# Kernel optimization log

Measured on AMD Instinct MI355X. Metric: run time of the kernel, lower is better.

## Reference

```python
import jax, jax.numpy as jnp
import numpy as np

B, HC, WC, KC = 4, 32, 32, 1024   # coarse feature map (ResNet101 layer3)
HF, WF, KF = 128, 128, 256        # fine feature map (ResNet101 layer1)
DC = 4                            # downscale_coef; HF // DC == HC


def setup_inputs() -> dict:
    key = jax.random.key(0)
    k1, k2, k3, k4 = jax.random.split(key, 4)
    return {
        "F_g1_coarse": jax.random.normal(k1, (B, HC, WC, KC), jnp.float32),
        "F_gk_coarse": jax.random.normal(k2, (B, HC, WC, KC), jnp.float32),
        "F_g1_fine": jax.random.normal(k3, (B, HF, WF, KF), jnp.float32),
        "F_gk_fine": jax.random.normal(k4, (B, HF, WF, KF), jnp.float32),
    }


def _coarse_match(f1, fk):
    # For every coarse position in Gk find nearest (L2) coarse position in G1.
    b, h, w, k = f1.shape
    a = f1.reshape(b, h * w, k)   # G1 positions
    q = fk.reshape(b, h * w, k)   # Gk positions
    # ||q||^2 + ||a||^2 - 2 q.a  -> [B, HW_gk, HW_g1]
    d = ((q * q).sum(-1)[:, :, None]
         + (a * a).sum(-1)[:, None, :]
         - 2.0 * jnp.einsum('bnk,bmk->bnm', q, a))
    idx = jnp.argmin(d, axis=-1)                       # [B, HW]
    cm = jnp.stack([idx // w, idx % w], axis=-1)       # (row, col) in G1
    return cm.reshape(b, h, w, 2).astype(jnp.int32)


def _fine_match(f1, fk, cm, dc):
    # Refine each dc x dc fine tile of Gk by searching the fine pixels of G1
    # covered by the coarse matches of the 3x3 coarse-neighborhood.
    b, h, w, k = fk.shape
    hc, wc = h // dc, w // dc
    off = jnp.arange(-1, 2)
    nI = jnp.clip(jnp.arange(hc)[:, None] + off[None, :], 0, hc - 1)  # [Hc,3]
    nJ = jnp.clip(jnp.arange(wc)[:, None] + off[None, :], 0, wc - 1)  # [Wc,3]
    # neighbor coarse matches: [B, Hc, Wc, 3, 3, 2]
    nb = cm[:, nI[:, None, :, None], nJ[None, :, None, :]]
    nb = nb.reshape(b, hc, wc, 9, 2)
    # expand each coarse match to its dc*dc fine pixels in G1
    sr = jnp.repeat(jnp.arange(dc), dc)   # [dc^2] row shifts
    sc = jnp.tile(jnp.arange(dc), dc)     # [dc^2] col shifts
    ncand = 9 * dc * dc                   # 144 candidates per tile
    cand_r = (nb[..., 0][..., None] * dc + sr).reshape(b, hc, wc, ncand)
    cand_c = (nb[..., 1][..., None] * dc + sc).reshape(b, hc, wc, ncand)
    # gather candidate fine features from G1: [B, Hc, Wc, N, K]
    bi = jnp.arange(b)[:, None, None, None]
    cand_f = f1[bi, cand_r, cand_c]
    # fine tile features of Gk: [B, Hc, Wc, dc^2, K]
    fkb = fk.reshape(b, hc, dc, wc, dc, k).transpose(0, 1, 3, 2, 4, 5)
    fkb = fkb.reshape(b, hc, wc, dc * dc, k)
    dist = ((fkb * fkb).sum(-1)[..., :, None]
            + (cand_f * cand_f).sum(-1)[..., None, :]
            - 2.0 * jnp.einsum('bhwpk,bhwnk->bhwpn', fkb, cand_f))
    best = jnp.argmin(dist, axis=-1)      # [B, Hc, Wc, dc^2]
    hi = jnp.arange(hc)[None, :, None, None]
    wi = jnp.arange(wc)[None, None, :, None]
    best_r = cand_r[bi, hi, wi, best]     # [B, Hc, Wc, dc^2]
    best_c = cand_c[bi, hi, wi, best]
    def to_grid(x):
        return x.reshape(b, hc, wc, dc, dc).transpose(0, 1, 3, 2, 4).reshape(b, h, w)
    return jnp.stack([to_grid(best_r), to_grid(best_c)], axis=-1).astype(jnp.int32)


def reference(F_g1_coarse, F_gk_coarse, F_g1_fine, F_gk_fine):
    closest_coarse = _coarse_match(F_g1_coarse, F_gk_coarse)   # [B,Hc,Wc,2]
    closest_fine = _fine_match(F_g1_fine, F_gk_fine, closest_coarse, DC)  # [B,H,W,2]
    return closest_coarse, closest_fine
```

## Files before the change

kernel.cpp:

```cpp
#include <hip/hip_runtime.h>
#include <cstdint>
#include <cstddef>

#define BB 4
#define HCC 32
#define WCC 32
#define KCC 1024
#define NCC (HCC*WCC)
#define HFF 128
#define WFF 128
#define KFF 256
#define DCC 4
#define NCHUNK 8

typedef _Float16 half8 __attribute__((ext_vector_type(8)));
typedef _Float16 half4_t __attribute__((ext_vector_type(4)));
typedef float f32x4 __attribute__((ext_vector_type(4)));
#define MFMA16(a,b,c) __builtin_amdgcn_mfma_f32_16x16x32_f16((a),(b),(c),0,0,0)
#define INV2K 0.00048828125f

__device__ inline void cvt8(const float4 u0, const float4 u1, half8& h, half8& l2) {
  float uu[8];
  *(float4*)uu = u0; *(float4*)(uu + 4) = u1;
  #pragma unroll
  for (int e = 0; e < 8; ++e) {
    _Float16 hh = (_Float16)uu[e];
    float r = (uu[e] - (float)hh) * 2048.0f;
    h[e] = hh; l2[e] = (_Float16)r;
  }
}

template<int K>
__global__ __launch_bounds__(256) void preconv_kernel(
    const float* __restrict__ src0, const float* __restrict__ src1,
    _Float16* __restrict__ hi0, _Float16* __restrict__ lo0,
    _Float16* __restrict__ hi1, _Float16* __restrict__ lo1,
    float* __restrict__ nr0, float* __restrict__ nr1, int rows) {
  const float* __restrict__ src = blockIdx.y ? src1 : src0;
  _Float16* __restrict__ hi = blockIdx.y ? hi1 : hi0;
  _Float16* __restrict__ lo = blockIdx.y ? lo1 : lo0;
  float* __restrict__ nrm = blockIdx.y ? nr1 : nr0;
  const int wave = threadIdx.x >> 6, lane = threadIdx.x & 63;
  const int row = blockIdx.x * 4 + wave;
  if (row >= rows) return;
  const float* p = src + (size_t)row * K;
  const size_t ob = (size_t)row * K + lane * 4;
  float s = 0.f;
  #pragma unroll
  for (int c = 0; c < K / 256; ++c) {
    float4 v = *(const float4*)(p + c * 256 + lane * 4);
    s += v.x*v.x + v.y*v.y + v.z*v.z + v.w*v.w;
    float vv[4] = {v.x, v.y, v.z, v.w};
    half4_t h, l2;
    #pragma unroll
    for (int e = 0; e < 4; ++e) {
      _Float16 hh = (_Float16)vv[e];
      l2[e] = (_Float16)((vv[e] - (float)hh) * 2048.0f);
      h[e] = hh;
    }
    *(half4_t*)(hi + ob + c * 256) = h;
    *(half4_t*)(lo + ob + c * 256) = l2;
  }
  #pragma unroll
  for (int m = 1; m <= 32; m <<= 1) s += __shfl_xor(s, m, 64);
  if (lane == 0) nrm[row] = s;
}

__global__ __launch_bounds__(256) void preconv_fine_kernel(
    const float* __restrict__ src, _Float16* __restrict__ hl,
    float* __restrict__ nrm, int rows) {
  const int wave = threadIdx.x >> 6, lane = threadIdx.x & 63;
  const int row = blockIdx.x * 4 + wave;
  if (row >= rows) return;
  float4 v = *(const float4*)(src + (size_t)row * KFF + lane * 4);
  float s = v.x*v.x + v.y*v.y + v.z*v.z + v.w*v.w;
  float vv[4] = {v.x, v.y, v.z, v.w};
  half4_t h, l2;
  #pragma unroll
  for (int e = 0; e < 4; ++e) {
    _Float16 hh = (_Float16)vv[e];
    l2[e] = (_Float16)((vv[e] - (float)hh) * 2048.0f);
    h[e] = hh;
  }
  const size_t dst = (size_t)row * 512 + (lane >> 3) * 64 + ((lane >> 1) & 3) * 16 + (lane & 1) * 4;
  *(half4_t*)(hl + dst)     = h;
  *(half4_t*)(hl + dst + 8) = l2;
  #pragma unroll
  for (int m = 1; m <= 32; m <<= 1) s += __shfl_xor(s, m, 64);
  if (lane == 0) nrm[row] = s;
}

__global__ __launch_bounds__(256) void coarse_kernel3(
    const _Float16* __restrict__ gAhi, const _Float16* __restrict__ gAlo,
    const _Float16* __restrict__ gBhi, const _Float16* __restrict__ gBlo,
    const float* __restrict__ na, const float* __restrict__ nq,
    float* __restrict__ pval, int* __restrict__ pidx) {
  __shared__ _Float16 Ahi[128][64], Alo[128][64];
  __shared__ _Float16 Bhi[64][64],  Blo[64][64];
  __shared__ float a2s[128], q2s[64];
  __shared__ float redv[2][64];
  __shared__ int   redi[2][64];

  const int t = threadIdx.x;
  const int chunk = blockIdx.x;
  const int n0 = blockIdx.y * 64;
  const int b  = blockIdx.z;
  const int m0 = chunk * 128;

  const int ar = t >> 1, ahf = t & 1;
  const int brw = t >> 2, bq = t & 3;
  const int l  = t & 63;
  const int wv = t >> 6;
  const int wm = wv >> 1, wn = wv & 1;

  if (t < 128) a2s[t] = na[b*NCC + m0 + t];
  else if (t < 192) q2s[t - 128] = nq[b*NCC + n0 + (t - 128)];

  const _Float16* __restrict__ gah = gAhi + (size_t)(b*NCC + m0 + ar) * KCC + ahf * 32;
  const _Float16* __restrict__ gal = gAlo + (size_t)(b*NCC + m0 + ar) * KCC + ahf * 32;
  const _Float16* __restrict__ gbh = gBhi + (size_t)(b*NCC + n0 + brw) * KCC + bq * 16;
  const _Float16* __restrict__ gbl = gBlo + (size_t)(b*NCC + n0 + brw) * KCC + bq * 16;

  f32x4 accA[4][2], accB[4][2];
  #pragma unroll
  for (int mt = 0; mt < 4; ++mt)
    #pragma unroll
    for (int nt = 0; nt < 2; ++nt) { accA[mt][nt] = (f32x4)0.f; accB[mt][nt] = (f32x4)0.f; }

  half8 pah[4], pal[4], pbh[2], pbl[2];
  #pragma unroll
  for (int c2 = 0; c2 < 4; ++c2) { pah[c2] = *(const half8*)(gah + c2*8); pal[c2] = *(const half8*)(gal + c2*8); }
  #pragma unroll
  for (int c2 = 0; c2 < 2; ++c2) { pbh[c2] = *(const half8*)(gbh + c2*8); pbl[c2] = *(const half8*)(gbl + c2*8); }

  for (int k0 = 0; k0 < KCC; k0 += 64) {
    __syncthreads();
    #pragma unroll
    for (int c2 = 0; c2 < 4; ++c2) {
      int cs = (ahf * 4 + c2) ^ (ar & 7);
      *(half8*)&Ahi[ar][cs * 8] = pah[c2];
      *(half8*)&Alo[ar][cs * 8] = pal[c2];
    }
    #pragma unroll
    for (int c2 = 0; c2 < 2; ++c2) {
      int cs = (bq * 2 + c2) ^ (brw & 7);
      *(half8*)&Bhi[brw][cs * 8] = pbh[c2];
      *(half8*)&Blo[brw][cs * 8] = pbl[c2];
    }
    __syncthreads();

    if (k0 + 64 < KCC) {
      #pragma unroll
      for (int c2 = 0; c2 < 4; ++c2) {
        pah[c2] = *(const half8*)(gah + k0 + 64 + c2*8);
        pal[c2] = *(const half8*)(gal + k0 + 64 + c2*8);
      }
      #pragma unroll
      for (int c2 = 0; c2 < 2; ++c2) {
        pbh[c2] = *(const half8*)(gbh + k0 + 64 + c2*8);
        pbl[c2] = *(const half8*)(gbl + k0 + 64 + c2*8);
      }
    }

    #pragma unroll
    for (int kk = 0; kk < 2; ++kk) {
      const int cs = ((kk * 4 + (l >> 4)) ^ (l & 7)) * 8;
      half8 ah[4], al[4], bh[2], bl[2];
      #pragma unroll
      for (int mt = 0; mt < 4; ++mt) {
        int row = wm * 64 + mt * 16 + (l & 15);
        ah[mt] = *(const half8*)&Ahi[row][cs];
        al[mt] = *(const half8*)&Alo[row][cs];
      }
      #pragma unroll
      for (int nt = 0; nt < 2; ++nt) {
        int row = wn * 32 + nt * 16 + (l & 15);
        bh[nt] = *(const half8*)&Bhi[row][cs];
        bl[nt] = *(const half8*)&Blo[row][cs];
      }
      #pragma unroll
      for (int mt = 0; mt < 4; ++mt)
        #pragma unroll
        for (int nt = 0; nt < 2; ++nt) {
          accA[mt][nt] = MFMA16(ah[mt], bh[nt], accA[mt][nt]);
          accB[mt][nt] = MFMA16(ah[mt], bl[nt], accB[mt][nt]);
          accB[mt][nt] = MFMA16(al[mt], bh[nt], accB[mt][nt]);
        }
    }
  }

  #pragma unroll
  for (int nt = 0; nt < 2; ++nt) {
    float q2 = q2s[wn * 32 + nt * 16 + (l & 15)];
    float bv = 3.0e38f; int bi = 0;
    #pragma unroll
    for (int mt = 0; mt < 4; ++mt)
      #pragma unroll
      for (int r = 0; r < 4; ++r) {
        float dot = accA[mt][nt][r] + accB[mt][nt][r] * INV2K;
        int ml = wm * 64 + mt * 16 + (l >> 4) * 4 + r;
        float d = (q2 + a2s[ml]) - 2.0f * dot;
        if (d < bv) { bv = d; bi = m0 + ml; }
      }
    #pragma unroll
    for (int mm = 16; mm < 64; mm <<= 1) {
      float ov = __shfl_xor(bv, mm, 64);
      int oi = __shfl_xor(bi, mm, 64);
      if (ov < bv || (ov == bv && oi < bi)) { bv = ov; bi = oi; }
    }
    if ((l >> 4) == 0) { redv[wm][wn*32 + nt*16 + l] = bv; redi[wm][wn*32 + nt*16 + l] = bi; }
  }
  __syncthreads();
  if (t < 64) {
    float v0 = redv[0][t]; int i0 = redi[0][t];
    float v1 = redv[1][t]; int i1 = redi[1][t];
    if (v1 < v0) { v0 = v1; i0 = i1; }
    pval[((size_t)b * NCC + n0 + t) * NCHUNK + chunk] = v0;
    pidx[((size_t)b * NCC + n0 + t) * NCHUNK + chunk] = i0;
  }
}

__global__ __launch_bounds__(256) void coarse_reduce_kernel(
    const float* __restrict__ pval, const int* __restrict__ pidx,
    int* __restrict__ out) {
  int g = blockIdx.x * 256 + threadIdx.x;
  if (g >= BB * NCC) return;
  float bv = pval[(size_t)g * NCHUNK];
  int bi = pidx[(size_t)g * NCHUNK];
  #pragma unroll
  for (int c = 1; c < NCHUNK; ++c) {
    float v = pval[(size_t)g * NCHUNK + c];
    int ix = pidx[(size_t)g * NCHUNK + c];
    if (v < bv) { bv = v; bi = ix; }
  }
  out[(size_t)g*2]     = bi >> 5;
  out[(size_t)g*2 + 1] = bi & 31;
}

__global__ __launch_bounds__(256) void fine_kernel8(
    const _Float16* __restrict__ gHL, const float* __restrict__ fkf,
    const float* __restrict__ naf, const int* __restrict__ coarse,
    int* __restrict__ outf) {
  __shared__ _Float16 CS[2][288 * 64];
  __shared__ int   rIdx[288];
  __shared__ float tNORM[288];
  __shared__ int cbr[18], cbc[18];

  const int t = threadIdx.x;
  const int bx = blockIdx.x, ii = blockIdx.y, b = blockIdx.z;
  const int l = t & 63, w = t >> 6;
  const int jj = bx * 4 + w;

  if (t < 18) {
    int wy = t / 6, wx = t % 6;
    int y = min(max(ii - 1 + wy, 0), HCC - 1);
    int x = min(max(bx * 4 - 1 + wx, 0), WCC - 1);
    int base = ((b * HCC + y) * WCC + x) * 2;
    cbr[t] = coarse[base]; cbc[t] = coarse[base + 1];
  }
  __syncthreads();
  for (int idx = t; idx < 288; idx += 256) {
    int slot = idx >> 4, s = idx & 15;
    int row = cbr[slot] * DCC + (s >> 2), col = cbc[slot] * DCC + (s & 3);
    int g = (b * HFF + row) * WFF + col;
    rIdx[idx] = g; tNORM[idx] = naf[g];
  }
  __syncthreads();

  unsigned srcOff[9], dstOff[9];
  #pragma unroll
  for (int it = 0; it < 9; ++it) {
    int g2 = it * 256 + t;
    int rowG = g2 >> 3, lc = g2 & 7;
    srcOff[it] = (unsigned)rIdx[rowG] * 512u + (unsigned)((lc >> 1) * 16 + (lc & 1) * 8);
    dstOff[it] = (unsigned)(rowG * 64 + (lc ^ (rowG & 7)) * 8);
  }

  const int q = l >> 4, r = l & 15;
  const int qfr = ii * DCC + (r >> 2), qfc = jj * DCC + (r & 3);
  const float* qsrc = fkf + ((size_t)(b * HFF + qfr) * WFF + qfc) * KFF + q * 8;

  half8 pf[9];
  #pragma unroll
  for (int it = 0; it < 9; ++it) pf[it] = *(const half8*)(gHL + srcOff[it]);
  #pragma unroll
  for (int it = 0; it < 9; ++it) *(half8*)&CS[0][dstOff[it]] = pf[it];
  #pragma unroll
  for (int it = 0; it < 9; ++it) pf[it] = *(const half8*)(gHL + srcOff[it] + 64u);
  float4 qu0 = *(const float4*)(qsrc);
  float4 qu1 = *(const float4*)(qsrc + 4);
  __syncthreads();

  f32x4 accA[9], accB[9];
  #pragma unroll
  for (int T = 0; T < 9; ++T) { accA[T] = (f32x4)0.f; accB[T] = (f32x4)0.f; }

  const int woff[9] = {0, 1, 2, 6, 7, 8, 12, 13, 14};
  const int wbase = w;
  const int rsw = r & 7;
  const int c0 = ((q * 2) ^ rsw) * 8, c1 = ((q * 2 + 1) ^ rsw) * 8;
  float qnp = 0.f;

  #pragma unroll
  for (int ke = 0; ke < 8; ++ke) {
    const int cur = ke & 1;
    qnp += qu0.x*qu0.x + qu0.y*qu0.y + qu0.z*qu0.z + qu0.w*qu0.w
         + qu1.x*qu1.x + qu1.y*qu1.y + qu1.z*qu1.z + qu1.w*qu1.w;
    half8 bh, bl;
    cvt8(qu0, qu1, bh, bl);
    if (ke < 7) {
      qu0 = *(const float4*)(qsrc + (ke + 1) * 32);
      qu1 = *(const float4*)(qsrc + (ke + 1) * 32 + 4);
    }
    #pragma unroll
    for (int T = 0; T < 9; ++T) {
      int rowG = (wbase + woff[T]) * 16 + r;
      half8 ah = *(const half8*)&CS[cur][rowG * 64 + c0];
      half8 al = *(const half8*)&CS[cur][rowG * 64 + c1];
      accA[T] = MFMA16(ah, bh, accA[T]);
      accB[T] = MFMA16(ah, bl, accB[T]);
      accB[T] = MFMA16(al, bh, accB[T]);
    }
    if (ke < 7) {
      #pragma unroll
      for (int it = 0; it < 9; ++it) *(half8*)&CS[cur ^ 1][dstOff[it]] = pf[it];
      if (ke < 6) {
        #pragma unroll
        for (int it = 0; it < 9; ++it)
          pf[it] = *(const half8*)(gHL + srcOff[it] + (unsigned)(ke + 2) * 64u);
      }
    }
    __syncthreads();
  }

  qnp += __shfl_xor(qnp, 16, 64);
  qnp += __shfl_xor(qnp, 32, 64);
  const float q2v = qnp;

  {
    float bv = 3.0e38f; int bi = 0;
    #pragma unroll
    for (int T = 0; T < 9; ++T) {
      int slot = wbase + woff[T];
      #pragma unroll
      for (int r2 = 0; r2 < 4; ++r2) {
        int s4 = q * 4 + r2;
        float cn = tNORM[slot * 16 + s4];
        float dot = accA[T][r2] + accB[T][r2] * INV2K;
        float d = (q2v + cn) - 2.0f * dot;
        int m = T * 16 + s4;
        if (d < bv) { bv = d; bi = m; }
      }
    }
    #pragma unroll
    for (int mm = 16; mm < 64; mm <<= 1) {
      float ov = __shfl_xor(bv, mm, 64);
      int oi = __shfl_xor(bi, mm, 64);
      if (ov < bv || (ov == bv && oi < bi)) { bv = ov; bi = oi; }
    }
    if (l < 16) {
      int T = bi >> 4, s3 = bi & 15, slot = wbase + woff[T];
      int br = cbr[slot] * DCC + (s3 >> 2);
      int bc = cbc[slot] * DCC + (s3 & 3);
      int fr = ii * DCC + (l >> 2), fc = jj * DCC + (l & 3);
      size_t ob = ((size_t)(b * HFF + fr) * WFF + fc) * 2;
      outf[ob]     = br;
      outf[ob + 1] = bc;
    }
  }
}

__global__ __launch_bounds__(256, 2) void coarse_kernel(
    const float* __restrict__ f1, const float* __restrict__ fk,
    float* __restrict__ pval, int* __restrict__ pidx) {
  __shared__ _Float16 Ahi[128][64], Alo[128][64];
  __shared__ _Float16 Bhi[64][64],  Blo[64][64];
  __shared__ float npA[256], npB[256];
  __shared__ float a2s[128], q2s[64];
  __shared__ float redv[2][64];
  __shared__ int   redi[2][64];

  const int t = threadIdx.x;
  const int chunk = blockIdx.x;
  const int n0 = blockIdx.y * 64;
  const int b  = blockIdx.z;
  const int m0 = chunk * 128;

  const float* __restrict__ Abase = f1 + ((size_t)b * NCC + m0) * KCC;
  const float* __restrict__ Bbase = fk + ((size_t)b * NCC + n0) * KCC;

  const int ar = t >> 1, ahf = t & 1;
  const int brw = t >> 2, bq = t & 3;
  const int l  = t & 63;
  const int wv = t >> 6;
  const int wm = wv >> 1, wn = wv & 1;

  float nrmA = 0.f, nrmB = 0.f;
  f32x4 accA[4][2], accB[4][2];
  #pragma unroll
  for (int mt = 0; mt < 4; ++mt)
    #pragma unroll
    for (int nt = 0; nt < 2; ++nt) { accA[mt][nt] = (f32x4)0.f; accB[mt][nt] = (f32x4)0.f; }

  for (int k0 = 0; k0 < KCC; k0 += 64) {
    __syncthreads();
    {
      const float4* src = (const float4*)(Abase + (size_t)ar * KCC + k0 + ahf * 32);
      float4 va[8];
      #pragma unroll
      for (int i2 = 0; i2 < 8; ++i2) va[i2] = src[i2];
      #pragma unroll
      for (int i2 = 0; i2 < 8; ++i2)
        nrmA += va[i2].x*va[i2].x + va[i2].y*va[i2].y + va[i2].z*va[i2].z + va[i2].w*va[i2].w;
      #pragma unroll
      for (int c2 = 0; c2 < 4; ++c2) {
        half8 hh, hl;
        cvt8(va[c2*2], va[c2*2+1], hh, hl);
        int cs = (ahf * 4 + c2) ^ (ar & 7);
        *(half8*)&Ahi[ar][cs * 8] = hh;
        *(half8*)&Alo[ar][cs * 8] = hl;
      }
    }
    {
      const float4* src = (const float4*)(Bbase + (size_t)brw * KCC + k0 + bq * 16);
      float4 vb[4];
      #pragma unroll
      for (int i2 = 0; i2 < 4; ++i2) vb[i2] = src[i2];
      #pragma unroll
      for (int i2 = 0; i2 < 4; ++i2)
        nrmB += vb[i2].x*vb[i2].x + vb[i2].y*vb[i2].y + vb[i2].z*vb[i2].z + vb[i2].w*vb[i2].w;
      #pragma unroll
      for (int c2 = 0; c2 < 2; ++c2) {
        half8 hh, hl;
        cvt8(vb[c2*2], vb[c2*2+1], hh, hl);
        int cs = (bq * 2 + c2) ^ (brw & 7);
        *(half8*)&Bhi[brw][cs * 8] = hh;
        *(half8*)&Blo[brw][cs * 8] = hl;
      }
    }
    __syncthreads();

    #pragma unroll
    for (int kk = 0; kk < 2; ++kk) {
      const int cs = ((kk * 4 + (l >> 4)) ^ (l & 7)) * 8;
      half8 ah[4], al[4], bh[2], bl[2];
      #pragma unroll
      for (int mt = 0; mt < 4; ++mt) {
        int rw = wm * 64 + mt * 16 + (l & 15);
        ah[mt] = *(const half8*)&Ahi[rw][cs];
        al[mt] = *(const half8*)&Alo[rw][cs];
      }
      #pragma unroll
      for (int nt = 0; nt < 2; ++nt) {
        int rw = wn * 32 + nt * 16 + (l & 15);
        bh[nt] = *(const half8*)&Bhi[rw][cs];
        bl[nt] = *(const half8*)&Blo[rw][cs];
      }
      #pragma unroll
      for (int mt = 0; mt < 4; ++mt)
        #pragma unroll
        for (int nt = 0; nt < 2; ++nt) {
          accA[mt][nt] = MFMA16(ah[mt], bh[nt], accA[mt][nt]);
          accB[mt][nt] = MFMA16(ah[mt], bl[nt], accB[mt][nt]);
          accB[mt][nt] = MFMA16(al[mt], bh[nt], accB[mt][nt]);
        }
    }
  }

  npA[t] = nrmA; npB[t] = nrmB;
  __syncthreads();
  if (t < 128) a2s[t] = npA[2*t] + npA[2*t + 1];
  if (t < 64)  q2s[t] = npB[4*t] + npB[4*t + 1] + npB[4*t + 2] + npB[4*t + 3];
  __syncthreads();

  #pragma unroll
  for (int nt = 0; nt < 2; ++nt) {
    float q2 = q2s[wn * 32 + nt * 16 + (l & 15)];
    float bv = 3.0e38f; int bi = 0;
    #pragma unroll
    for (int mt = 0; mt < 4; ++mt)
      #pragma unroll
      for (int r = 0; r < 4; ++r) {
        float dot = accA[mt][nt][r] + accB[mt][nt][r] * INV2K;
        int ml = wm * 64 + mt * 16 + (l >> 4) * 4 + r;
        float d = (q2 + a2s[ml]) - 2.0f * dot;
        if (d < bv) { bv = d; bi = m0 + ml; }
      }
    #pragma unroll
    for (int mm = 16; mm < 64; mm <<= 1) {
      float ov = __shfl_xor(bv, mm, 64);
      int oi = __shfl_xor(bi, mm, 64);
      if (ov < bv || (ov == bv && oi < bi)) { bv = ov; bi = oi; }
    }
    if ((l >> 4) == 0) { redv[wm][wn*32 + nt*16 + l] = bv; redi[wm][wn*32 + nt*16 + l] = bi; }
  }
  __syncthreads();
  if (t < 64) {
    float v0 = redv[0][t]; int i0 = redi[0][t];
    float v1 = redv[1][t]; int i1 = redi[1][t];
    if (v1 < v0) { v0 = v1; i0 = i1; }
    pval[((size_t)b * NCC + n0 + t) * NCHUNK + chunk] = v0;
    pidx[((size_t)b * NCC + n0 + t) * NCHUNK + chunk] = i0;
  }
}

__global__ __launch_bounds__(192) void fine_kernel(
    const float* __restrict__ f1, const float* __restrict__ fkf,
    const int* __restrict__ coarse, int* __restrict__ outf) {
  __shared__ _Float16 Qhi[16][256], Qlo[16][256];
  __shared__ float qn[16], cn[144];
  __shared__ int cROW[144];
  __shared__ int cbr[9], cbc[9];
  __shared__ float redv[3][16];
  __shared__ int   redi[3][16];

  const int t = threadIdx.x;
  const int j = blockIdx.x, i = blockIdx.y, b = blockIdx.z;
  const int l = t & 63, wv = t >> 6;

  if (t < 9) {
    int di = t / 3 - 1, dj = t % 3 - 1;
    int y = min(max(i + di, 0), HCC - 1);
    int x = min(max(j + dj, 0), WCC - 1);
    int base = ((b*HCC + y)*WCC + x) * 2;
    cbr[t] = coarse[base];
    cbc[t] = coarse[base + 1];
  }
  __syncthreads();
  if (t < 144) {
    int n9 = t >> 4, s = t & 15;
    int row = cbr[n9]*DCC + (s >> 2), col = cbc[n9]*DCC + (s & 3);
    cROW[t] = (b*HFF + row)*WFF + col;
  }
  if (t < 64) {
    int qr = l & 15, qq = l >> 4;
    int fr = i*DCC + (qr >> 2), fc = j*DCC + (qr & 3);
    const float* src = fkf + ((size_t)(b*HFF + fr)*WFF + fc) * KFF + qq * 64;
    float s2 = 0.f;
    #pragma unroll
    for (int c2 = 0; c2 < 8; ++c2) {
      float4 u0 = *(const float4*)(src + c2*8);
      float4 u1 = *(const float4*)(src + c2*8 + 4);
      s2 += u0.x*u0.x + u0.y*u0.y + u0.z*u0.z + u0.w*u0.w
          + u1.x*u1.x + u1.y*u1.y + u1.z*u1.z + u1.w*u1.w;
      half8 hh, hl;
      cvt8(u0, u1, hh, hl);
      int cs = (qq * 8 + c2) ^ (qr & 7);
      *(half8*)&Qhi[qr][cs * 8] = hh;
      *(half8*)&Qlo[qr][cs * 8] = hl;
    }
    s2 += __shfl_xor(s2, 16, 64);
    s2 += __shfl_xor(s2, 32, 64);
    if (qq == 0) qn[qr] = s2;
  }
  __syncthreads();

  const float* ap[3];
  #pragma unroll
  for (int T = 0; T < 3; ++T)
    ap[T] = f1 + (size_t)cROW[(wv*3 + T)*16 + (l & 15)] * KFF;

  f32x4 accA[3], accB[3];
  float nrmp[3];
  #pragma unroll
  for (int T = 0; T < 3; ++T) { accA[T] = (f32x4)0.f; accB[T] = (f32x4)0.f; nrmp[T] = 0.f; }

  #pragma unroll 2
  for (int s = 0; s < 8; ++s) {
    const int cs = ((s * 4 + (l >> 4)) ^ (l & 7)) * 8;
    half8 bh = *(const half8*)&Qhi[l & 15][cs];
    half8 bl = *(const half8*)&Qlo[l & 15][cs];
    #pragma unroll
    for (int T = 0; T < 3; ++T) {
      const float* p = ap[T] + s*32 + (l >> 4)*8;
      float4 u0 = *(const float4*)p;
      float4 u1 = *(const float4*)(p + 4);
      nrmp[T] += u0.x*u0.x + u0.y*u0.y + u0.z*u0.z + u0.w*u0.w
               + u1.x*u1.x + u1.y*u1.y + u1.z*u1.z + u1.w*u1.w;
      half8 ahv, alv;
      cvt8(u0, u1, ahv, alv);
      accA[T] = MFMA16(ahv, bh, accA[T]);
      accB[T] = MFMA16(ahv, bl, accB[T]);
      accB[T] = MFMA16(alv, bh, accB[T]);
    }
  }

  #pragma unroll
  for (int T = 0; T < 3; ++T) {
    float np = nrmp[T];
    np += __shfl_xor(np, 16, 64);
    np += __shfl_xor(np, 32, 64);
    if ((l >> 4) == 0) cn[(wv*3 + T)*16 + l] = np;
  }
  __syncthreads();

  {
    float q2 = qn[l & 15];
    float bv = 3.0e38f; int bi = 0;
    #pragma unroll
    for (int T = 0; T < 3; ++T)
      #pragma unroll
      for (int r = 0; r < 4; ++r) {
        float dot = accA[T][r] + accB[T][r] * INV2K;
        int m = (wv*3 + T)*16 + (l >> 4)*4 + r;
        float d = (q2 + cn[m]) - 2.0f * dot;
        if (d < bv) { bv = d; bi = m; }
      }
    #pragma unroll
    for (int mm = 16; mm < 64; mm <<= 1) {
      float ov = __shfl_xor(bv, mm, 64);
      int oi = __shfl_xor(bi, mm, 64);
      if (ov < bv || (ov == bv && oi < bi)) { bv = ov; bi = oi; }
    }
    if ((l >> 4) == 0 && l < 16) { redv[wv][l] = bv; redi[wv][l] = bi; }
  }
  __syncthreads();

  if (t < 16) {
    float v = redv[0][t]; int ix = redi[0][t];
    #pragma unroll
    for (int w = 1; w < 3; ++w) {
      float ov = redv[w][t];
      if (ov < v) { v = ov; ix = redi[w][t]; }
    }
    int n9 = ix >> 4, s3 = ix & 15;
    int br = cbr[n9]*DCC + (s3 >> 2);
    int bc = cbc[n9]*DCC + (s3 & 3);
    int fr = i*DCC + (t >> 2), fc = j*DCC + (t & 3);
    size_t ob = ((size_t)(b*HFF + fr)*WFF + fc) * 2;
    outf[ob]     = br;
    outf[ob + 1] = bc;
  }
}

extern "C" void kernel_launch(void* const* d_in, const int* in_sizes, int n_in,
                              void* d_out, int out_size, void* d_ws, size_t ws_size,
                              hipStream_t stream) {
  (void)in_sizes; (void)n_in; (void)out_size;
  const float* f1c = (const float*)d_in[0];
  const float* fkc = (const float*)d_in[1];
  const float* f1f = (const float*)d_in[2];
  const float* fkf = (const float*)d_in[3];
  int* out = (int*)d_out;

  const size_t NEED = 101220352;
  if (ws_size >= NEED) {
    char* w = (char*)d_ws;
    _Float16* cAhi = (_Float16*)(w);
    _Float16* cAlo = (_Float16*)(w + 8388608);
    _Float16* cBhi = (_Float16*)(w + 16777216);
    _Float16* cBlo = (_Float16*)(w + 25165824);
    _Float16* fHL  = (_Float16*)(w + 33554432);
    float* na_c = (float*)(w + 100663296);
    float* nq_c = (float*)(w + 100679680);
    float* na_f = (float*)(w + 100696064);
    float* pval = (float*)(w + 100958208);
    int*   pidx = (int*)  (w + 101089280);

    preconv_kernel<KCC><<<dim3(BB*NCC/4, 2), 256, 0, stream>>>(
        f1c, fkc, cAhi, cAlo, cBhi, cBlo, na_c, nq_c, BB*NCC);
    preconv_fine_kernel<<<dim3(BB*HFF*WFF/4), 256, 0, stream>>>(
        f1f, fHL, na_f, BB*HFF*WFF);
    coarse_kernel3<<<dim3(NCHUNK, NCC/64, BB), 256, 0, stream>>>(
        cAhi, cAlo, cBhi, cBlo, na_c, nq_c, pval, pidx);
    coarse_reduce_kernel<<<dim3((BB*NCC + 255)/256), 256, 0, stream>>>(pval, pidx, out);
    fine_kernel8<<<dim3(WCC/4, HCC, BB), 256, 0, stream>>>(
        fHL, fkf, na_f, out, out + BB*NCC*2);
  } else {
    float* pval = (float*)d_ws;
    int*   pidx = (int*)((float*)d_ws + BB*NCC*NCHUNK);
    coarse_kernel<<<dim3(NCHUNK, NCC/64, BB), 256, 0, stream>>>(f1c, fkc, pval, pidx);
    coarse_reduce_kernel<<<dim3((BB*NCC + 255)/256), 256, 0, stream>>>(pval, pidx, out);
    fine_kernel<<<dim3(WCC, HCC, BB), 192, 0, stream>>>(f1f, fkf, out, out + BB*NCC*2);
  }
}
```

Before: 105.8 us.

## Fuse fine-feature preconversion into coarse GEMM kernel and raise MFMA priority

Merges the fine-map fp16 hi/lo preconversion into the coarse matching kernel as a horizontally fused grid. Every third block does coarse GEMM work and the other two convert 64 fine rows each, so the memory-bound conversion overlaps the MFMA-bound coarse GEMM and one launch is removed. It also wraps the MFMA loops in the coarse and fine kernels with s_setprio to favour matrix issue. The coarse reduce kernel now takes the chunk count as a runtime argument, which drops the unrolled loop. The risk is that mixed block types share LDS allocation and occupancy limits, so conversion blocks reserve the coarse kernel's shared memory.

Result: slower. 120.3 us (+13.7%).

```diff
diff --git a/kernel.cpp b/kernel.cpp
--- a/kernel.cpp
+++ b/kernel.cpp
@@ -90,21 +90,51 @@
   if (lane == 0) nrm[row] = s;
 }
 
-__global__ __launch_bounds__(256) void coarse_kernel3(
+__global__ __launch_bounds__(256) void coarse_pf_kernel(
     const _Float16* __restrict__ gAhi, const _Float16* __restrict__ gAlo,
     const _Float16* __restrict__ gBhi, const _Float16* __restrict__ gBlo,
     const float* __restrict__ na, const float* __restrict__ nq,
-    float* __restrict__ pval, int* __restrict__ pidx) {
+    float* __restrict__ pval, int* __restrict__ pidx,
+    const float* __restrict__ f1f, _Float16* __restrict__ fHL,
+    float* __restrict__ na_f) {
   __shared__ _Float16 Ahi[128][64], Alo[128][64];
   __shared__ _Float16 Bhi[64][64],  Blo[64][64];
   __shared__ float a2s[128], q2s[64];
   __shared__ float redv[2][64];
   __shared__ int   redi[2][64];
 
+  const int id = blockIdx.x;
   const int t = threadIdx.x;
-  const int chunk = blockIdx.x;
-  const int n0 = blockIdx.y * 64;
-  const int b  = blockIdx.z;
+
+  if (id % 3 != 0) {
+    const int pid = (id / 3) * 2 + (id % 3) - 1;
+    const int wave = t >> 6, lane = t & 63;
+    for (int row = pid * 64 + wave; row < pid * 64 + 64; row += 4) {
+      float4 v = *(const float4*)(f1f + (size_t)row * KFF + lane * 4);
+      float s = v.x*v.x + v.y*v.y + v.z*v.z + v.w*v.w;
+      float vv[4] = {v.x, v.y, v.z, v.w};
+      half4_t h, l2;
+      #pragma unroll
+      for (int e = 0; e < 4; ++e) {
+        _Float16 hh = (_Float16)vv[e];
+        l2[e] = (_Float16)((vv[e] - (float)hh) * 2048.0f);
+        h[e] = hh;
+      }
+      const size_t dst = (size_t)row * 512 + (lane >> 3) * 64 + ((lane >> 1) & 3) * 16 + (lane & 1) * 4;
+      *(half4_t*)(fHL + dst)     = h;
+      *(half4_t*)(fHL + dst + 8) = l2;
+      float s2 = s;
+      #pragma unroll
+      for (int m = 1; m <= 32; m <<= 1) s2 += __shfl_xor(s2, m, 64);
+      if (lane == 0) na_f[row] = s2;
+    }
+    return;
+  }
+
+  const int cid = id / 3;
+  const int chunk = cid & 7;
+  const int n0 = ((cid >> 3) & 15) * 64;
+  const int b  = cid >> 7;
   const int m0 = chunk * 128;
 
   const int ar = t >> 1, ahf = t & 1;
@@ -178,6 +208,7 @@
         bh[nt] = *(const half8*)&Bhi[row][cs];
         bl[nt] = *(const half8*)&Blo[row][cs];
       }
+      __builtin_amdgcn_s_setprio(1);
       #pragma unroll
       for (int mt = 0; mt < 4; ++mt)
         #pragma unroll
@@ -186,6 +217,7 @@
           accB[mt][nt] = MFMA16(ah[mt], bl[nt], accB[mt][nt]);
           accB[mt][nt] = MFMA16(al[mt], bh[nt], accB[mt][nt]);
         }
+      __builtin_amdgcn_s_setprio(0);
     }
   }
 
@@ -222,15 +254,14 @@
 
 __global__ __launch_bounds__(256) void coarse_reduce_kernel(
     const float* __restrict__ pval, const int* __restrict__ pidx,
-    int* __restrict__ out) {
+    int* __restrict__ out, int nchunk) {
   int g = blockIdx.x * 256 + threadIdx.x;
   if (g >= BB * NCC) return;
-  float bv = pval[(size_t)g * NCHUNK];
-  int bi = pidx[(size_t)g * NCHUNK];
-  #pragma unroll
-  for (int c = 1; c < NCHUNK; ++c) {
-    float v = pval[(size_t)g * NCHUNK + c];
-    int ix = pidx[(size_t)g * NCHUNK + c];
+  float bv = pval[(size_t)g * nchunk];
+  int bi = pidx[(size_t)g * nchunk];
+  for (int c = 1; c < nchunk; ++c) {
+    float v = pval[(size_t)g * nchunk + c];
+    int ix = pidx[(size_t)g * nchunk + c];
     if (v < bv) { bv = v; bi = ix; }
   }
   out[(size_t)g*2]     = bi >> 5;
@@ -312,6 +343,7 @@
       qu0 = *(const float4*)(qsrc + (ke + 1) * 32);
       qu1 = *(const float4*)(qsrc + (ke + 1) * 32 + 4);
     }
+    __builtin_amdgcn_s_setprio(1);
     #pragma unroll
     for (int T = 0; T < 9; ++T) {
       int rowG = (wbase + woff[T]) * 16 + r;
@@ -321,6 +353,7 @@
       accB[T] = MFMA16(ah, bl, accB[T]);
       accB[T] = MFMA16(al, bh, accB[T]);
     }
+    __builtin_amdgcn_s_setprio(0);
     if (ke < 7) {
       #pragma unroll
       for (int it = 0; it < 9; ++it) *(half8*)&CS[cur ^ 1][dstOff[it]] = pf[it];
@@ -659,18 +692,18 @@
 
     preconv_kernel<KCC><<<dim3(BB*NCC/4, 2), 256, 0, stream>>>(
         f1c, fkc, cAhi, cAlo, cBhi, cBlo, na_c, nq_c, BB*NCC);
-    preconv_fine_kernel<<<dim3(BB*HFF*WFF/4), 256, 0, stream>>>(
-        f1f, fHL, na_f, BB*HFF*WFF);
-    coarse_kernel3<<<dim3(NCHUNK, NCC/64, BB), 256, 0, stream>>>(
-        cAhi, cAlo, cBhi, cBlo, na_c, nq_c, pval, pidx);
-    coarse_reduce_kernel<<<dim3((BB*NCC + 255)/256), 256, 0, stream>>>(pval, pidx, out);
+    coarse_pf_kernel<<<dim3(1536), 256, 0, stream>>>(
+        cAhi, cAlo, cBhi, cBlo, na_c, nq_c, pval, pidx, f1f, fHL, na_f);
+    coarse_reduce_kernel<<<dim3((BB*NCC + 255)/256), 256, 0, stream>>>(
+        pval, pidx, out, NCHUNK);
     fine_kernel8<<<dim3(WCC/4, HCC, BB), 256, 0, stream>>>(
         fHL, fkf, na_f, out, out + BB*NCC*2);
   } else {
     float* pval = (float*)d_ws;
     int*   pidx = (int*)((float*)d_ws + BB*NCC*NCHUNK);
     coarse_kernel<<<dim3(NCHUNK, NCC/64, BB), 256, 0, stream>>>(f1c, fkc, pval, pidx);
-    coarse_reduce_kernel<<<dim3((BB*NCC + 255)/256), 256, 0, stream>>>(pval, pidx, out);
+    coarse_reduce_kernel<<<dim3((BB*NCC + 255)/256), 256, 0, stream>>>(
+        pval, pidx, out, NCHUNK);
     fine_kernel<<<dim3(WCC, HCC, BB), 192, 0, stream>>>(f1f, fkf, out, out + BB*NCC*2);
   }
 }
```
